# Kernel optimization log

Measured on AMD Instinct MI355X. Metric: run time of the kernel, lower is better.

The kernel has to match this reference:

```python
import jax, jax.numpy as jnp
import numpy as np

N = 32768   # num nodes == num edges (forced by concat in forward)
I = 128     # input_size
H = 128     # hidden_size
O = 128     # output_size
R = 2       # num_relations


def _lstm_seq(x, Wih, Whh, bih, bhh):
    """PyTorch-style single-layer LSTM over an unbatched sequence x [T, D]."""
    xg = x @ Wih.T + (bih + bhh)  # precompute input projection [T, 4H]
    Hh = Whh.shape[1]

    def step(carry, xgt):
        h, c = carry
        g = xgt + h @ Whh.T
        i, f, gg, o = jnp.split(g, 4)
        i = jax.nn.sigmoid(i)
        f = jax.nn.sigmoid(f)
        gg = jnp.tanh(gg)
        o = jax.nn.sigmoid(o)
        c = f * c + i * gg
        h = o * jnp.tanh(c)
        return (h, c), h

    h0 = jnp.zeros((Hh,), x.dtype)
    (_, _), hs = jax.lax.scan(step, (h0, h0), xg)
    return hs  # [T, H]


def setup_inputs() -> dict:
    key = jax.random.key(0)
    ks = jax.random.split(key, 12)
    s = 0.05
    inputs = jax.random.normal(ks[0], (N, I), dtype=jnp.float32)
    edges = jax.random.randint(ks[1], (N, 2), 0, N, dtype=jnp.int64)
    in_W = jax.random.normal(ks[2], (H, I), dtype=jnp.float32) * s
    in_b = jax.random.normal(ks[3], (H,), dtype=jnp.float32) * s
    out_W = jax.random.normal(ks[4], (O, H), dtype=jnp.float32) * s
    out_b = jax.random.normal(ks[5], (O,), dtype=jnp.float32) * s
    edge_W = jax.random.normal(ks[6], (R, H, 2 * H), dtype=jnp.float32) * s
    edge_b = jax.random.normal(ks[7], (R, H), dtype=jnp.float32) * s
    lstm_Wih = jax.random.normal(ks[8], (R, 4 * H, I + H), dtype=jnp.float32) * s
    lstm_Whh = jax.random.normal(ks[9], (R, 4 * H, H), dtype=jnp.float32) * s
    lstm_bih = jax.random.normal(ks[10], (R, 4 * H), dtype=jnp.float32) * s
    lstm_bhh = jax.random.normal(ks[11], (R, 4 * H), dtype=jnp.float32) * s
    return {
        "inputs": inputs, "edges": edges,
        "in_W": in_W, "in_b": in_b, "out_W": out_W, "out_b": out_b,
        "edge_W": edge_W, "edge_b": edge_b,
        "lstm_Wih": lstm_Wih, "lstm_Whh": lstm_Whh,
        "lstm_bih": lstm_bih, "lstm_bhh": lstm_bhh,
    }


def reference(inputs, edges, in_W, in_b, out_W, out_b,
              edge_W, edge_b, lstm_Wih, lstm_Whh, lstm_bih, lstm_bhh):
    nodes = inputs @ in_W.T + in_b  # [N, H]
    src = edges[:, 0]
    dst = edges[:, 1]
    for r in range(edge_W.shape[0]):
        # gather node pairs, edge MLP
        pair = jnp.concatenate([nodes[src], nodes[dst]], axis=1)  # [N, 2H]
        edge_h = pair @ edge_W[r].T + edge_b[r]                    # [N, H]
        # LSTM over node sequence on [inputs ; edge_h]
        x = jnp.concatenate([inputs, edge_h], axis=1)              # [N, I+H]
        nodes = _lstm_seq(x, lstm_Wih[r], lstm_Whh[r], lstm_bih[r], lstm_bhh[r])
    return nodes @ out_W.T + out_b  # [N, O]
```

## Files before the change

### kernel.cpp

```cpp
#include <hip/hip_runtime.h>
#include <hip/hip_bf16.h>
#include <cstddef>

#define NN 32768
#define BM 64
#define BN 64
#define BK 32

typedef float f32x4 __attribute__((ext_vector_type(4)));
typedef short short8 __attribute__((ext_vector_type(8)));

__device__ inline unsigned short f2bf(float f) {
    unsigned u = __builtin_bit_cast(unsigned, f);
    unsigned r = (u + 0x7FFFu + ((u >> 16) & 1u)) >> 16;
    return (unsigned short)r;
}
__device__ inline float sigmoid_f(float x) {
    float e = __expf(-x);
    return __builtin_amdgcn_rcpf(1.f + e);
}
__device__ inline float tanh_f(float x) {
    float e = __expf(-2.f * x);
    return 2.f * __builtin_amdgcn_rcpf(1.f + e) - 1.f;
}

__device__ inline int permrow(int p) {
    return ((p >> 4) & 3) * 128 + ((p >> 6) << 4) + (p & 15);
}

__global__ __launch_bounds__(256) void gemm_cat(
    const float* __restrict__ A1, const int* __restrict__ idx1,
    const float* __restrict__ A2, const int* __restrict__ idx2, int istr,
    int K1, int K2,
    const float* __restrict__ W, const float* __restrict__ b1,
    const float* __restrict__ b2, int permW,
    float* __restrict__ C, int M, int N)
{
    const int K = K1 + K2;
    __shared__ __align__(16) float As[BK][BM + 4];
    __shared__ __align__(16) float Ws[BK][BN + 4];
    const int tid = threadIdx.x;
    const int m0 = blockIdx.x * BM;
    const int n0 = blockIdx.y * BN;
    const int tx = tid & 15;
    const int ty = tid >> 4;
    float acc[4][4] = {};

    for (int k0 = 0; k0 < K; k0 += BK) {
        #pragma unroll
        for (int p = 0; p < 2; ++p) {
            int q = tid + p * 256;
            int row = q >> 3;
            int kq = (q & 7) * 4;
            int gk = k0 + kq;
            int grow = m0 + row;
            const float* src;
            if (gk < K1) {
                int r = idx1 ? idx1[grow * istr] : grow;
                src = A1 + (size_t)r * K1 + gk;
            } else {
                int r = idx2 ? idx2[grow * istr] : grow;
                src = A2 + (size_t)r * K2 + (gk - K1);
            }
            float4 v = *(const float4*)src;
            As[kq + 0][row] = v.x; As[kq + 1][row] = v.y;
            As[kq + 2][row] = v.z; As[kq + 3][row] = v.w;
        }
        #pragma unroll
        for (int p = 0; p < 2; ++p) {
            int q = tid + p * 256;
            int row = q >> 3;
            int kq = (q & 7) * 4;
            int wrow = n0 + row;
            if (permW) wrow = permrow(wrow);
            const float* src = W + (size_t)wrow * K + (k0 + kq);
            float4 v = *(const float4*)src;
            Ws[kq + 0][row] = v.x; Ws[kq + 1][row] = v.y;
            Ws[kq + 2][row] = v.z; Ws[kq + 3][row] = v.w;
        }
        __syncthreads();
        #pragma unroll
        for (int kk = 0; kk < BK; ++kk) {
            float4 a = *(const float4*)&As[kk][ty * 4];
            float4 b = *(const float4*)&Ws[kk][tx * 4];
            float av[4] = {a.x, a.y, a.z, a.w};
            float bv[4] = {b.x, b.y, b.z, b.w};
            #pragma unroll
            for (int i = 0; i < 4; ++i)
                #pragma unroll
                for (int jj = 0; jj < 4; ++jj)
                    acc[i][jj] += av[i] * bv[jj];
        }
        __syncthreads();
    }
    #pragma unroll
    for (int i = 0; i < 4; ++i) {
        int gr = m0 + ty * 4 + i;
        #pragma unroll
        for (int jj = 0; jj < 4; ++jj) {
            int gc = n0 + tx * 4 + jj;
            int bi = permW ? permrow(gc) : gc;
            float bias = b1 ? b1[bi] : 0.f;
            if (b2) bias += b2[bi];
            C[(size_t)gr * N + gc] = acc[i][jj] + bias;
        }
    }
}

__global__ __launch_bounds__(512)
__attribute__((amdgpu_waves_per_eu(2, 2)))
void lstm_scan(const float* __restrict__ xg,
               const float* __restrict__ Whh,
               float* __restrict__ hs,
               int T)
{
    __shared__ __align__(16) unsigned short hbuf[2][128];
    const int tid  = threadIdx.x;
    const int w    = tid >> 6;
    const int lane = tid & 63;
    const int m    = lane & 15;
    const int grp  = lane >> 4;

    short8 wfrag[4][4];
    #pragma unroll
    for (int nt = 0; nt < 4; ++nt)
        #pragma unroll
        for (int kt = 0; kt < 4; ++kt) {
            const float* src = Whh + (size_t)(nt * 128 + w * 16 + m) * 128
                                   + kt * 32 + grp * 8;
            f32x4 v0 = *(const f32x4*)src;
            f32x4 v1 = *(const f32x4*)(src + 4);
            short8 s;
            s[0] = (short)f2bf(v0[0]); s[1] = (short)f2bf(v0[1]);
            s[2] = (short)f2bf(v0[2]); s[3] = (short)f2bf(v0[3]);
            s[4] = (short)f2bf(v1[0]); s[5] = (short)f2bf(v1[1]);
            s[6] = (short)f2bf(v1[2]); s[7] = (short)f2bf(v1[3]);
            wfrag[nt][kt] = s;
        }

    if (tid < 128) { hbuf[0][tid] = 0; hbuf[1][tid] = 0; }

    const int xoff = w * 64 + m;
    float xcA[4], xcB[4];
    #pragma unroll
    for (int nt = 0; nt < 4; ++nt) {
        xcA[nt] = xg[xoff + nt * 16];
        xcB[nt] = xg[512 + xoff + nt * 16];
    }
    const float* xpre = xg + 2 * 512 + xoff;
    float* hsp = hs + w * 16 + m;
    float c = 0.f;
    f32x4 acc[4];
    #pragma unroll
    for (int nt = 0; nt < 4; ++nt) acc[nt] = (f32x4){0.f, 0.f, 0.f, 0.f};
    __syncthreads();

    for (int t = 0; t < T; t += 2) {
        {
            short8 hfrag[4];
            #pragma unroll
            for (int kt = 0; kt < 4; ++kt)
                hfrag[kt] = *(const short8*)&hbuf[0][kt * 32 + grp * 8];

            #pragma unroll
            for (int nt = 0; nt < 4; ++nt) acc[nt][0] = xcA[nt];

            if (t + 2 < T) {
                #pragma unroll
                for (int nt = 0; nt < 4; ++nt) xcA[nt] = xpre[nt * 16];
            }

            #pragma unroll
            for (int kt = 0; kt < 4; ++kt)
                #pragma unroll
                for (int nt = 0; nt < 4; ++nt)
                    acc[nt] = __builtin_amdgcn_mfma_f32_16x16x32_bf16(
                        hfrag[kt], wfrag[nt][kt], acc[nt], 0, 0, 0);

            float iv = sigmoid_f(acc[0][0]);
            float fv = sigmoid_f(acc[1][0]);
            float gv = tanh_f   (acc[2][0]);
            float ov = sigmoid_f(acc[3][0]);
            c = fv * c + iv * gv;
            float h = ov * tanh_f(c);

            if (grp == 0) {
                hbuf[1][w * 16 + m] = f2bf(h);
                hsp[0] = h;
            }
            __syncthreads();
        }
        {
            short8 hfrag[4];
            #pragma unroll
            for (int kt = 0; kt < 4; ++kt)
                hfrag[kt] = *(const short8*)&hbuf[1][kt * 32 + grp * 8];

            #pragma unroll
            for (int nt = 0; nt < 4; ++nt) acc[nt][0] = xcB[nt];

            if (t + 3 < T) {
                #pragma unroll
                for (int nt = 0; nt < 4; ++nt) xcB[nt] = xpre[512 + nt * 16];
            }

            #pragma unroll
            for (int kt = 0; kt < 4; ++kt)
                #pragma unroll
                for (int nt = 0; nt < 4; ++nt)
                    acc[nt] = __builtin_amdgcn_mfma_f32_16x16x32_bf16(
                        hfrag[kt], wfrag[nt][kt], acc[nt], 0, 0, 0);

            float iv = sigmoid_f(acc[0][0]);
            float fv = sigmoid_f(acc[1][0]);
            float gv = tanh_f   (acc[2][0]);
            float ov = sigmoid_f(acc[3][0]);
            c = fv * c + iv * gv;
            float h = ov * tanh_f(c);

            if (grp == 0) {
                hbuf[0][w * 16 + m] = f2bf(h);
                hsp[128] = h;
            }
            __syncthreads();
        }
        xpre += 1024;
        hsp  += 256;
    }
}

extern "C" void kernel_launch(void* const* d_in, const int* in_sizes, int n_in,
                              void* d_out, int out_size, void* d_ws, size_t ws_size,
                              hipStream_t stream) {
    const float* inputs = (const float*)d_in[0];
    const int*   edges  = (const int*)d_in[1];
    const float* in_W   = (const float*)d_in[2];
    const float* in_b   = (const float*)d_in[3];
    const float* out_W  = (const float*)d_in[4];
    const float* out_b  = (const float*)d_in[5];
    const float* edge_W = (const float*)d_in[6];
    const float* edge_b = (const float*)d_in[7];
    const float* Wih    = (const float*)d_in[8];
    const float* Whh    = (const float*)d_in[9];
    const float* bih    = (const float*)d_in[10];
    const float* bhh    = (const float*)d_in[11];
    float* out = (float*)d_out;

    float* ws = (float*)d_ws;
    float* nodesA = ws;
    float* nodesB = nodesA + (size_t)NN * 128;
    float* edge_h = nodesB + (size_t)NN * 128;
    float* xgbuf  = edge_h + (size_t)NN * 128;

    dim3 blk(256);
    dim3 g128(NN / BM, 128 / BN);
    dim3 g512(NN / BM, 512 / BN);

    gemm_cat<<<g128, blk, 0, stream>>>(inputs, nullptr, nullptr, nullptr, 1,
                                       128, 0, in_W, in_b, nullptr, 0,
                                       nodesA, NN, 128);

    const float* cur = nodesA;
    float* nxt = nodesB;
    for (int r = 0; r < 2; ++r) {
        gemm_cat<<<g128, blk, 0, stream>>>(cur, edges + 0, cur, edges + 1, 2,
                                           128, 128,
                                           edge_W + (size_t)r * 128 * 256,
                                           edge_b + (size_t)r * 128, nullptr, 0,
                                           edge_h, NN, 128);
        gemm_cat<<<g512, blk, 0, stream>>>(inputs, nullptr, edge_h, nullptr, 1,
                                           128, 128,
                                           Wih + (size_t)r * 512 * 256,
                                           bih + (size_t)r * 512,
                                           bhh + (size_t)r * 512, 1,
                                           xgbuf, NN, 512);
        lstm_scan<<<1, 512, 0, stream>>>(xgbuf, Whh + (size_t)r * 512 * 128,
                                         nxt, NN);
        const float* tmp = cur;
        cur = nxt;
        nxt = (float*)tmp;
    }

    gemm_cat<<<g128, blk, 0, stream>>>(cur, nullptr, nullptr, nullptr, 1,
                                       128, 0, out_W, out_b, nullptr, 0,
                                       out, NN, 128);
}
```

Measured before the change: 30.19 ms.

## Split LSTM gate activations across lane groups and use a lighter LDS barrier

Each 16-lane group in the scan wave now computes only one gate's activation, where before every lane evaluated all four, and the results are exchanged with two xor-shuffles. Each lane loads one precomputed input-projection value per step instead of four. __syncthreads is replaced by an inline s_waitcnt lgkmcnt(0) plus s_barrier so the barrier does not also wait on outstanding global stores. This shortens the serial per-step critical path of the recurrence, at the cost of cross-lane shuffle latency and relying on the hand-written barrier being sufficient for ordering.

Measured after the change: 32.49 ms. 7.6% more time.

```diff
diff --git a/kernel.cpp b/kernel.cpp
--- a/kernel.cpp
+++ b/kernel.cpp
@@ -14,10 +14,6 @@
     unsigned u = __builtin_bit_cast(unsigned, f);
     unsigned r = (u + 0x7FFFu + ((u >> 16) & 1u)) >> 16;
     return (unsigned short)r;
-}
-__device__ inline float sigmoid_f(float x) {
-    float e = __expf(-x);
-    return __builtin_amdgcn_rcpf(1.f + e);
 }
 __device__ inline float tanh_f(float x) {
     float e = __expf(-2.f * x);
@@ -107,6 +103,8 @@
     }
 }
 
+#define LDS_BARRIER() asm volatile("s_waitcnt lgkmcnt(0)\n\ts_barrier" ::: "memory")
+
 __global__ __launch_bounds__(512)
 __attribute__((amdgpu_waves_per_eu(2, 2)))
 void lstm_scan(const float* __restrict__ xg,
@@ -140,19 +138,20 @@
 
     if (tid < 128) { hbuf[0][tid] = 0; hbuf[1][tid] = 0; }
 
-    const int xoff = w * 64 + m;
-    float xcA[4], xcB[4];
-    #pragma unroll
-    for (int nt = 0; nt < 4; ++nt) {
-        xcA[nt] = xg[xoff + nt * 16];
-        xcB[nt] = xg[512 + xoff + nt * 16];
-    }
+    const int xoff = w * 64 + grp * 16 + m;
+    float xcA = xg[xoff];
+    float xcB = xg[512 + xoff];
     const float* xpre = xg + 2 * 512 + xoff;
     float* hsp = hs + w * 16 + m;
     float c = 0.f;
     f32x4 acc[4];
     #pragma unroll
     for (int nt = 0; nt < 4; ++nt) acc[nt] = (f32x4){0.f, 0.f, 0.f, 0.f};
+
+    const bool isg    = (grp == 2);
+    const bool hiGrp  = (grp >= 2);
+    const bool oddGrp = (grp & 1);
+    const float amul  = isg ? 2.f : 1.f;
     __syncthreads();
 
     for (int t = 0; t < T; t += 2) {
@@ -163,12 +162,9 @@
                 hfrag[kt] = *(const short8*)&hbuf[0][kt * 32 + grp * 8];
 
             #pragma unroll
-            for (int nt = 0; nt < 4; ++nt) acc[nt][0] = xcA[nt];
-
-            if (t + 2 < T) {
-                #pragma unroll
-                for (int nt = 0; nt < 4; ++nt) xcA[nt] = xpre[nt * 16];
-            }
+            for (int nt = 0; nt < 4; ++nt) acc[nt][0] = xcA;
+
+            if (t + 2 < T) xcA = xpre[0];
 
             #pragma unroll
             for (int kt = 0; kt < 4; ++kt)
@@ -177,10 +173,23 @@
                     acc[nt] = __builtin_amdgcn_mfma_f32_16x16x32_bf16(
                         hfrag[kt], wfrag[nt][kt], acc[nt], 0, 0, 0);
 
-            float iv = sigmoid_f(acc[0][0]);
-            float fv = sigmoid_f(acc[1][0]);
-            float gv = tanh_f   (acc[2][0]);
-            float ov = sigmoid_f(acc[3][0]);
+            float e01 = oddGrp ? acc[1][0] : acc[0][0];
+            float e23 = oddGrp ? acc[3][0] : acc[2][0];
+            float gown = hiGrp ? e23 : e01;
+            float ee = __expf(-amul * gown);
+            float ss = __builtin_amdgcn_rcpf(1.f + ee);
+            float act = isg ? 2.f * ss - 1.f : ss;
+
+            float p16 = __shfl_xor(act, 16);
+            float lo = oddGrp ? p16 : act;
+            float hi = oddGrp ? act : p16;
+            float lo2 = __shfl_xor(lo, 32);
+            float hi2 = __shfl_xor(hi, 32);
+            float iv = hiGrp ? lo2 : lo;
+            float gv = hiGrp ? lo  : lo2;
+            float fv = hiGrp ? hi2 : hi;
+            float ov = hiGrp ? hi  : hi2;
+
             c = fv * c + iv * gv;
             float h = ov * tanh_f(c);
 
@@ -188,7 +197,7 @@
                 hbuf[1][w * 16 + m] = f2bf(h);
                 hsp[0] = h;
             }
-            __syncthreads();
+            LDS_BARRIER();
         }
         {
             short8 hfrag[4];
@@ -197,12 +206,9 @@
                 hfrag[kt] = *(const short8*)&hbuf[1][kt * 32 + grp * 8];
 
             #pragma unroll
-            for (int nt = 0; nt < 4; ++nt) acc[nt][0] = xcB[nt];
-
-            if (t + 3 < T) {
-                #pragma unroll
-                for (int nt = 0; nt < 4; ++nt) xcB[nt] = xpre[512 + nt * 16];
-            }
+            for (int nt = 0; nt < 4; ++nt) acc[nt][0] = xcB;
+
+            if (t + 3 < T) xcB = xpre[512];
 
             #pragma unroll
             for (int kt = 0; kt < 4; ++kt)
@@ -211,10 +217,23 @@
                     acc[nt] = __builtin_amdgcn_mfma_f32_16x16x32_bf16(
                         hfrag[kt], wfrag[nt][kt], acc[nt], 0, 0, 0);
 
-            float iv = sigmoid_f(acc[0][0]);
-            float fv = sigmoid_f(acc[1][0]);
-            float gv = tanh_f   (acc[2][0]);
-            float ov = sigmoid_f(acc[3][0]);
+            float e01 = oddGrp ? acc[1][0] : acc[0][0];
+            float e23 = oddGrp ? acc[3][0] : acc[2][0];
+            float gown = hiGrp ? e23 : e01;
+            float ee = __expf(-amul * gown);
+            float ss = __builtin_amdgcn_rcpf(1.f + ee);
+            float act = isg ? 2.f * ss - 1.f : ss;
+
+            float p16 = __shfl_xor(act, 16);
+            float lo = oddGrp ? p16 : act;
+            float hi = oddGrp ? act : p16;
+            float lo2 = __shfl_xor(lo, 32);
+            float hi2 = __shfl_xor(hi, 32);
+            float iv = hiGrp ? lo2 : lo;
+            float gv = hiGrp ? lo  : lo2;
+            float fv = hiGrp ? hi2 : hi;
+            float ov = hiGrp ? hi  : hi2;
+
             c = fv * c + iv * gv;
             float h = ov * tanh_f(c);
 
@@ -222,7 +241,7 @@
                 hbuf[0][w * 16 + m] = f2bf(h);
                 hsp[128] = h;
             }
-            __syncthreads();
+            LDS_BARRIER();
         }
         xpre += 1024;
         hsp  += 256;
```
